# Optimization experiments

Measured on AMD Instinct MI355X. Metric: run time of the kernel, lower is better.

The kernel has to match this reference:

```python
import jax, jax.numpy as jnp
import numpy as np

TS = 1.5          # hard-coded sampling period in forward()
W_CENTER = 337.927  # hard-coded center frequency in forward()


def shg_mat(yta):
    """Vectorized createSHGmat: yta is a complex64 vector of length N.
    Row m: Ts * fftshift(fft(fftshift(yta * roll(yta, delay[m]) * shiftFactor))).
    torch.roll(x, s)[j] == x[(j - s) % N], matching the gather below."""
    N = yta.shape[0]
    delays_f = jnp.arange(-(N // 2), N // 2, dtype=jnp.float32)
    delays_i = jnp.arange(-(N // 2), N // 2, dtype=jnp.int32)
    shift_factor = jnp.exp(-1j * 2.0 * W_CENTER * TS * delays_f).astype(jnp.complex64)  # [N]
    idx = (jnp.arange(N, dtype=jnp.int32)[None, :] - delays_i[:, None]) % N  # [N, N]
    y_shift = yta[idx]                                    # [N(delay), N(elem)]
    prod = yta[None, :] * y_shift * shift_factor[None, :]  # elementwise, [N, N]
    prod = jnp.fft.fftshift(prod, axes=-1)
    mat = TS * jnp.fft.fftshift(jnp.fft.fft(prod, axis=-1), axes=-1)
    return mat  # complex64 [N, N]


def frog_error(Tref, Tmeas):
    """calcFrogError: scalar FROG error between reference and measured traces."""
    mu = jnp.sum(Tmeas @ Tref) / jnp.sum(Tref @ Tref)
    r = jnp.sum((Tmeas - mu * Tref) ** 2)
    norm = jnp.float32(Tmeas.size) * jnp.max(Tmeas) ** 2
    return jnp.sqrt(r / norm)


def setup_inputs() -> dict:
    key = jax.random.key(0)
    k1, k2, k3 = jax.random.split(key, 3)
    B, N = 8, 1024
    prediction = jax.random.normal(k1, (B, 2 * N), dtype=jnp.float32)
    label = jax.random.normal(k2, (B, 2 * N), dtype=jnp.float32)
    spectrogram = jax.random.uniform(k3, (N, N), dtype=jnp.float32)
    return {"prediction": prediction, "label": label, "spectrogram": spectrogram}


def reference(prediction, label, spectrogram):
    B, two_n = prediction.shape
    n = two_n // 2
    pred_analytical = (prediction[:, :n] + 1j * prediction[:, n:]).astype(jnp.complex64)  # [B, N]
    mats = jax.vmap(shg_mat)(pred_analytical)          # [B, N, N] complex64
    Tref = jnp.abs(mats)                               # predicted SHG trace magnitude
    errs = jax.vmap(lambda t: frog_error(t, spectrogram))(Tref)  # [B]
    # loss = (sum over batch of frog_error) / batch_size; masked MSE terms in the
    # original are computed but never added to the returned loss, so they are omitted.
    return jnp.mean(errs)
```

## Files before the change

kernel.cpp:

```cpp
#include <hip/hip_runtime.h>
#include <math.h>

#define N 1024
#define B_ 8
#define T_ 512
#define NREP 4
#define CHUNKS 64

#define OFF_SF      0
#define OFF_TA      2048
#define OFF_TB      4096
#define OFF_ROWSUM  4224
#define ZERO_START  12416
#define OFF_COLSUMM 12416
#define OFF_SUMM2   13440
#define OFF_MAXM    13441
#define OFF_SUMMT   13448
#define OFF_SUMTT   13456
#define OFF_COLT    13464
#define WS_END      (OFF_COLT + B_ * NREP * N)

typedef float f2 __attribute__((ext_vector_type(2)));
__device__ __forceinline__ f2 mkf2(float a, float b) { f2 r; r.x = a; r.y = b; return r; }

__device__ __forceinline__ f2 cmulv(f2 a, f2 b) {
    f2 p = mkf2(a.x, a.x) * b;
    f2 q = mkf2(a.y, a.y) * mkf2(b.y, b.x);
    return mkf2(p.x - q.x, p.y + q.y);
}

__device__ __forceinline__ void dft4v(f2& a0, f2& a1, f2& a2, f2& a3) {
    f2 e0 = a0 + a2, e1 = a0 - a2, e2 = a1 + a3, e3 = a1 - a3;
    a0 = e0 + e2;
    a2 = e0 - e2;
    a1 = mkf2(e1.x + e3.y, e1.y - e3.x);
    a3 = mkf2(e1.x - e3.y, e1.y + e3.x);
}

__device__ __forceinline__ void dft16v(f2 x[16]) {
    #pragma unroll
    for (int b = 0; b < 4; ++b) dft4v(x[b], x[4 + b], x[8 + b], x[12 + b]);
    const float C1 = 0.9238795325112867f, S1 = 0.3826834323650898f;
    const float C2 = 0.7071067811865476f;
    x[5]  = cmulv(x[5],  mkf2( C1, -S1));
    x[6]  = cmulv(x[6],  mkf2( C2, -C2));
    x[7]  = cmulv(x[7],  mkf2( S1, -C1));
    x[9]  = cmulv(x[9],  mkf2( C2, -C2));
    x[10] = mkf2(x[10].y, -x[10].x);
    x[11] = cmulv(x[11], mkf2(-C2, -C2));
    x[13] = cmulv(x[13], mkf2( S1, -C1));
    x[14] = cmulv(x[14], mkf2(-C2, -C2));
    x[15] = cmulv(x[15], mkf2(-C1,  S1));
    #pragma unroll
    for (int c = 0; c < 4; ++c) dft4v(x[4*c], x[4*c+1], x[4*c+2], x[4*c+3]);
}

__device__ __forceinline__ float wave_sum(float v) {
    #pragma unroll
    for (int o = 32; o > 0; o >>= 1) v += __shfl_down(v, o, 64);
    return v;
}
__device__ __forceinline__ float wave_max(float v) {
    #pragma unroll
    for (int o = 32; o > 0; o >>= 1) v = fmaxf(v, __shfl_down(v, o, 64));
    return v;
}

template<int CTRL>
__device__ __forceinline__ float dppf(float x) {
    return __int_as_float(__builtin_amdgcn_update_dpp(
        0, __float_as_int(x), CTRL, 0xF, 0xF, true));
}
#define DPP_XOR1 0xB1
#define DPP_XOR2 0x4E

__global__ __launch_bounds__(256) void k_prep(float* ws) {
    const int e = blockIdx.x * 256 + threadIdx.x;
    if (e < 1024) {
        double ang = -2.0 * 337.927 * 1.5 * (double)(e - 512);
        double s, c;
        sincos(ang, &s, &c);
        ws[OFF_SF + 2 * e]     = (float)c;
        ws[OFF_SF + 2 * e + 1] = (float)s;
    } else if (e < 2048) {
        int e2 = e - 1024;
        int k1 = e2 >> 6, uu = e2 & 63;
        double ang = -2.0 * M_PI * (double)(uu * k1) / 1024.0;
        double s, c;
        sincos(ang, &s, &c);
        ws[OFF_TA + 2 * e2]     = (float)c;
        ws[OFF_TA + 2 * e2 + 1] = (float)s;
    } else if (e < 2112) {
        int e2 = e - 2048;
        int k2 = e2 >> 2, n3 = e2 & 3;
        double ang = -2.0 * M_PI * (double)(n3 * k2) / 64.0;
        double s, c;
        sincos(ang, &s, &c);
        ws[OFF_TB + 2 * e2]     = (float)c;
        ws[OFF_TB + 2 * e2 + 1] = (float)s;
    }
}

__global__ __attribute__((amdgpu_flat_work_group_size(T_, T_), amdgpu_waves_per_eu(2, 4)))
void k_row(const float* __restrict__ pred,
           const float* __restrict__ M,
           float* __restrict__ ws) {
    __shared__ f2   Y2[N];
    __shared__ f2   Ysf[N];
    __shared__ f2   taL[N];
    __shared__ f2   TPh[8][N / 2];
    __shared__ f2   TB2[64];
    __shared__ float colAcc[N];
    __shared__ float redf[2][8];
    const int t = threadIdx.x;
    const int cnk = blockIdx.x;
    const int y = blockIdx.y;
    const int wid = t >> 6, u = t & 63;

    if (y == 0) {
        const int r0 = cnk * 16;
        float cs0 = 0.f, cs1 = 0.f, sq = 0.f, mx = 0.f;
        for (int r = 0; r < 16; ++r) {
            const float* row = M + (size_t)(r0 + r) * N;
            float v0 = row[t], v1 = row[t + 512];
            cs0 += v0; cs1 += v1;
            sq += v0 * v0 + v1 * v1;
            mx = fmaxf(mx, fmaxf(v0, v1));
        }
        atomicAdd(&ws[OFF_COLSUMM + t],       cs0);
        atomicAdd(&ws[OFF_COLSUMM + t + 512], cs1);
        sq = wave_sum(sq);
        mx = wave_max(mx);
        if (u == 0) { redf[0][wid] = sq; redf[1][wid] = mx; }
        __syncthreads();
        if (t == 0) {
            float ssq = 0.f, smx = 0.f;
            #pragma unroll
            for (int i = 0; i < 8; ++i) { ssq += redf[0][i]; smx = fmaxf(smx, redf[1][i]); }
            atomicAdd(&ws[OFF_SUMM2], ssq);
            atomicMax((unsigned int*)ws + OFF_MAXM, __float_as_uint(smx));
        }
        return;
    }
    const int b = y - 1;

    {
        const float* pr = pred + (size_t)b * 2 * N;
        float2 re = *(const float2*)(pr + 2 * t);
        float2 im = *(const float2*)(pr + N + 2 * t);
        const f2* g = (const f2*)ws;
        f2 y0 = mkf2(re.x, im.x), y1 = mkf2(re.y, im.y);
        Y2[2 * t]     = y0;
        Y2[2 * t + 1] = y1;
        Ysf[2 * t]     = cmulv(y0, g[OFF_SF / 2 + 2 * t]);
        Ysf[2 * t + 1] = cmulv(y1, g[OFF_SF / 2 + 2 * t + 1]);
        taL[t]       = g[OFF_TA / 2 + t];
        taL[t + 512] = g[OFF_TA / 2 + t + 512];
        if (t < 64) TB2[t] = g[OFF_TB / 2 + t];
        colAcc[t] = 0.f;
        colAcc[t + 512] = 0.f;
    }
    __syncthreads();

    const int k1u = u >> 2;
    const int n3 = u & 3;
    const int k3 = ((u & 1) << 1) | ((u >> 1) & 1);
    const int clane = (k1u | (k3 << 8)) ^ 512;
    const bool hi2 = (u & 2) != 0;
    const bool odd = (u & 1) != 0;
    f2* tp = TPh[wid];

    float mtl = 0.f, ttl = 0.f;
    const int nrow = (cnk == 0 && wid == 0) ? 2 : 1;

    for (int rr = 0; rr < nrow; ++rr) {
        const int m = (rr == 0) ? (cnk * 8 + wid) : 512;
        const int mm = (N - m) & (N - 1);
        const bool domm = (mm != m);
        const float w = domm ? 2.f : 1.f;
        const float mmw = domm ? 1.f : 0.f;

        f2 x[16];
        const int sbase = (u - m + 512) & (N - 1);
        #pragma unroll
        for (int n1 = 0; n1 < 16; ++n1) {
            int j = (n1 << 6) + u;
            int s = (sbase + (n1 << 6)) & (N - 1);
            x[n1] = cmulv(Ysf[j], Y2[s]);
        }
        dft16v(x);
        #pragma unroll
        for (int r = 1; r < 16; ++r) {
            int k1 = ((r & 3) << 2) | (r >> 2);
            x[r] = cmulv(x[r], taL[(k1 << 6) + u]);
        }

        const float* Mrow  = M + (size_t)m * N + clane;
        const float* Mrow2 = M + (size_t)mm * N + clane;
        float mrA[16], mrB[16];
        #pragma unroll
        for (int r = 0; r < 16; ++r) {
            int k2 = ((r & 3) << 2) | (r >> 2);
            mrA[r] = Mrow[k2 << 4];
        }
        if (domm) {
            #pragma unroll
            for (int r = 0; r < 16; ++r) {
                int k2 = ((r & 3) << 2) | (r >> 2);
                mrB[r] = Mrow2[k2 << 4];
            }
        } else {
            #pragma unroll
            for (int r = 0; r < 16; ++r) mrB[r] = 0.f;
        }

        f2 yv[16];
        asm volatile("s_waitcnt lgkmcnt(0)" ::: "memory");
        #pragma unroll
        for (int r = 0; r < 16; ++r) if ((r & 3) < 2) {
            int k1 = ((r & 3) << 2) | (r >> 2);
            int el = ((k1 & 7) << 6) | (((k1u ^ k1) & 15) << 2) | n3;
            tp[el] = x[r];
        }
        asm volatile("s_waitcnt lgkmcnt(0)" ::: "memory");
        if (u < 32) {
            #pragma unroll
            for (int n2 = 0; n2 < 16; ++n2) {
                int el = ((k1u & 7) << 6) | (((n2 ^ k1u) & 15) << 2) | n3;
                yv[n2] = tp[el];
            }
        }
        asm volatile("s_waitcnt lgkmcnt(0)" ::: "memory");
        #pragma unroll
        for (int r = 0; r < 16; ++r) if ((r & 3) >= 2) {
            int k1 = ((r & 3) << 2) | (r >> 2);
            int el = ((k1 & 7) << 6) | (((k1u ^ k1) & 15) << 2) | n3;
            tp[el] = x[r];
        }
        asm volatile("s_waitcnt lgkmcnt(0)" ::: "memory");
        if (u >= 32) {
            #pragma unroll
            for (int n2 = 0; n2 < 16; ++n2) {
                int el = ((k1u & 7) << 6) | (((n2 ^ k1u) & 15) << 2) | n3;
                yv[n2] = tp[el];
            }
        }

        dft16v(yv);
        #pragma unroll
        for (int r = 1; r < 16; ++r) {
            int k2 = ((r & 3) << 2) | (r >> 2);
            yv[r] = cmulv(yv[r], TB2[(k2 << 2) | n3]);
        }

        const float w225 = w * 2.25f;
        float rs = 0.f;
        #pragma unroll
        for (int r = 0; r < 16; ++r) {
            int k2 = ((r & 3) << 2) | (r >> 2);
            float ar = yv[r].x, ai = yv[r].y;
            float br = dppf<DPP_XOR2>(ar), bi = dppf<DPP_XOR2>(ai);
            float zr = hi2 ? (br - ar) : (ar + br);
            float zi = hi2 ? (bi - ai) : (ai + bi);
            float qr = dppf<DPP_XOR1>(zr), qi = dppf<DPP_XOR1>(zi);
            float Xr = odd ? (qr - (hi2 ? zi : zr)) : (zr + (hi2 ? qi : qr));
            float Xi = odd ? (qi + (hi2 ? zr : -zi)) : (zi + (hi2 ? -qr : qi));
            float mag2 = Xr * Xr + Xi * Xi;
            float v = 1.5f * sqrtf(mag2);
            rs  += v;
            ttl += w225 * mag2;
            float ms = mrA[r] + mmw * mrB[r];
            mtl += ms * v;
            int cc = clane + (k2 << 4);
            atomicAdd(&colAcc[cc ^ ((cc >> 4) & 16)], w * v);
        }
        rs = wave_sum(rs);
        if (u == 0) {
            ws[OFF_ROWSUM + (size_t)b * N + m] = rs;
            if (domm) ws[OFF_ROWSUM + (size_t)b * N + mm] = rs;
        }
    }

    mtl = wave_sum(mtl);
    ttl = wave_sum(ttl);
    if (u == 0) { redf[0][wid] = mtl; redf[1][wid] = ttl; }
    __syncthreads();
    if (t == 0) {
        float smt = 0.f, stt = 0.f;
        #pragma unroll
        for (int i = 0; i < 8; ++i) { smt += redf[0][i]; stt += redf[1][i]; }
        atomicAdd(&ws[OFF_SUMMT + b], smt);
        atomicAdd(&ws[OFF_SUMTT + b], stt);
    }
    {
        float* colT = ws + OFF_COLT + (size_t)(b * NREP + (cnk & (NREP - 1))) * N;
        int j = t;
        atomicAdd(&colT[j], colAcc[j ^ ((j >> 4) & 16)]);
        j = t + 512;
        atomicAdd(&colT[j], colAcc[j ^ ((j >> 4) & 16)]);
    }
}

__global__ __launch_bounds__(256) void k_final(float* ws, float* out) {
    __shared__ double redn[4], redd[4];
    const int b = blockIdx.x;
    const int t = threadIdx.x;
    const int wid = t >> 6, lane = t & 63;
    const float* rowsum = ws + OFF_ROWSUM + (size_t)b * N;
    double num = 0.0, den = 0.0;
    #pragma unroll
    for (int q = 0; q < 4; ++q) {
        int j = t + 256 * q;
        double r = (double)rowsum[j];
        float ct = 0.f;
        #pragma unroll
        for (int rep = 0; rep < NREP; ++rep)
            ct += ws[OFF_COLT + (size_t)(b * NREP + rep) * N + j];
        num += (double)ws[OFF_COLSUMM + j] * r;
        den += (double)ct * r;
    }
    #pragma unroll
    for (int o = 32; o > 0; o >>= 1) {
        num += __shfl_down(num, o, 64);
        den += __shfl_down(den, o, 64);
    }
    if (lane == 0) { redn[wid] = num; redd[wid] = den; }
    __syncthreads();
    if (t == 0) {
        double NUM = redn[0] + redn[1] + redn[2] + redn[3];
        double DEN = redd[0] + redd[1] + redd[2] + redd[3];
        double mu = NUM / DEN;
        double r = (double)ws[OFF_SUMM2] - 2.0 * mu * (double)ws[OFF_SUMMT + b]
                 + mu * mu * (double)ws[OFF_SUMTT + b];
        float mx = ws[OFF_MAXM];
        double norm = 1048576.0 * (double)mx * (double)mx;
        atomicAdd(out, (float)(sqrt(r / norm) / 8.0));
    }
}

extern "C" void kernel_launch(void* const* d_in, const int* in_sizes, int n_in,
                              void* d_out, int out_size, void* d_ws, size_t ws_size,
                              hipStream_t stream) {
    const float* pred = (const float*)d_in[0];
    const float* M = (const float*)d_in[2];
    float* ws = (float*)d_ws;
    float* out = (float*)d_out;

    hipMemsetAsync(ws + ZERO_START, 0, (size_t)(WS_END - ZERO_START) * sizeof(float), stream);
    hipMemsetAsync(out, 0, sizeof(float), stream);
    k_prep<<<9, 256, 0, stream>>>(ws);
    dim3 grid(CHUNKS, B_ + 1);
    k_row<<<grid, T_, 0, stream>>>(pred, M, ws);
    k_final<<<B_, 256, 0, stream>>>(ws, out);
}
```

Before: 107.2 us.

## Fold spectrogram statistics into compute blocks and defer M row loads

Removes the dedicated y==0 block row that computed spectrogram column sums, sum of squares and max. Each of the 512 compute blocks now handles two spectrogram rows at its tail, so the statistics work is spread evenly instead of running in 64 separate blocks. The per-row M loads also move from before the second DFT stage into the magnitude loop, which removes 32 live registers but exposes global load latency at the point of use.

```diff
diff --git a/kernel.cpp b/kernel.cpp
--- a/kernel.cpp
+++ b/kernel.cpp
@@ -114,35 +114,8 @@
     __shared__ float redf[2][8];
     const int t = threadIdx.x;
     const int cnk = blockIdx.x;
-    const int y = blockIdx.y;
+    const int b = blockIdx.y;
     const int wid = t >> 6, u = t & 63;
-
-    if (y == 0) {
-        const int r0 = cnk * 16;
-        float cs0 = 0.f, cs1 = 0.f, sq = 0.f, mx = 0.f;
-        for (int r = 0; r < 16; ++r) {
-            const float* row = M + (size_t)(r0 + r) * N;
-            float v0 = row[t], v1 = row[t + 512];
-            cs0 += v0; cs1 += v1;
-            sq += v0 * v0 + v1 * v1;
-            mx = fmaxf(mx, fmaxf(v0, v1));
-        }
-        atomicAdd(&ws[OFF_COLSUMM + t],       cs0);
-        atomicAdd(&ws[OFF_COLSUMM + t + 512], cs1);
-        sq = wave_sum(sq);
-        mx = wave_max(mx);
-        if (u == 0) { redf[0][wid] = sq; redf[1][wid] = mx; }
-        __syncthreads();
-        if (t == 0) {
-            float ssq = 0.f, smx = 0.f;
-            #pragma unroll
-            for (int i = 0; i < 8; ++i) { ssq += redf[0][i]; smx = fmaxf(smx, redf[1][i]); }
-            atomicAdd(&ws[OFF_SUMM2], ssq);
-            atomicMax((unsigned int*)ws + OFF_MAXM, __float_as_uint(smx));
-        }
-        return;
-    }
-    const int b = y - 1;
 
     {
         const float* pr = pred + (size_t)b * 2 * N;
@@ -195,25 +168,6 @@
             x[r] = cmulv(x[r], taL[(k1 << 6) + u]);
         }
 
-        const float* Mrow  = M + (size_t)m * N + clane;
-        const float* Mrow2 = M + (size_t)mm * N + clane;
-        float mrA[16], mrB[16];
-        #pragma unroll
-        for (int r = 0; r < 16; ++r) {
-            int k2 = ((r & 3) << 2) | (r >> 2);
-            mrA[r] = Mrow[k2 << 4];
-        }
-        if (domm) {
-            #pragma unroll
-            for (int r = 0; r < 16; ++r) {
-                int k2 = ((r & 3) << 2) | (r >> 2);
-                mrB[r] = Mrow2[k2 << 4];
-            }
-        } else {
-            #pragma unroll
-            for (int r = 0; r < 16; ++r) mrB[r] = 0.f;
-        }
-
         f2 yv[16];
         asm volatile("s_waitcnt lgkmcnt(0)" ::: "memory");
         #pragma unroll
@@ -253,6 +207,8 @@
             yv[r] = cmulv(yv[r], TB2[(k2 << 2) | n3]);
         }
 
+        const float* Mrow  = M + (size_t)m * N + clane;
+        const float* Mrow2 = M + (size_t)mm * N + clane;
         const float w225 = w * 2.25f;
         float rs = 0.f;
         #pragma unroll
@@ -269,7 +225,7 @@
             float v = 1.5f * sqrtf(mag2);
             rs  += v;
             ttl += w225 * mag2;
-            float ms = mrA[r] + mmw * mrB[r];
+            float ms = Mrow[k2 << 4] + mmw * Mrow2[k2 << 4];
             mtl += ms * v;
             int cc = clane + (k2 << 4);
             atomicAdd(&colAcc[cc ^ ((cc >> 4) & 16)], w * v);
@@ -298,6 +254,30 @@
         atomicAdd(&colT[j], colAcc[j ^ ((j >> 4) & 16)]);
         j = t + 512;
         atomicAdd(&colT[j], colAcc[j ^ ((j >> 4) & 16)]);
+    }
+
+    {
+        const int gid = b * CHUNKS + cnk;
+        const float* s0 = M + (size_t)(2 * gid) * N;
+        const float* s1 = s0 + N;
+        float a0 = s0[t], a1 = s0[t + 512];
+        float b0 = s1[t], b1 = s1[t + 512];
+        atomicAdd(&ws[OFF_COLSUMM + t],       a0 + b0);
+        atomicAdd(&ws[OFF_COLSUMM + t + 512], a1 + b1);
+        float sq = a0 * a0 + a1 * a1 + b0 * b0 + b1 * b1;
+        float mx = fmaxf(fmaxf(a0, a1), fmaxf(b0, b1));
+        sq = wave_sum(sq);
+        mx = wave_max(mx);
+        __syncthreads();
+        if (u == 0) { redf[0][wid] = sq; redf[1][wid] = mx; }
+        __syncthreads();
+        if (t == 0) {
+            float ssq = 0.f, smx = 0.f;
+            #pragma unroll
+            for (int i = 0; i < 8; ++i) { ssq += redf[0][i]; smx = fmaxf(smx, redf[1][i]); }
+            atomicAdd(&ws[OFF_SUMM2], ssq);
+            atomicMax((unsigned int*)ws + OFF_MAXM, __float_as_uint(smx));
+        }
     }
 }
 
@@ -349,7 +329,7 @@
     hipMemsetAsync(ws + ZERO_START, 0, (size_t)(WS_END - ZERO_START) * sizeof(float), stream);
     hipMemsetAsync(out, 0, sizeof(float), stream);
     k_prep<<<9, 256, 0, stream>>>(ws);
-    dim3 grid(CHUNKS, B_ + 1);
+    dim3 grid(CHUNKS, B_);
     k_row<<<grid, T_, 0, stream>>>(pred, M, ws);
     k_final<<<B_, 256, 0, stream>>>(ws, out);
 }
```

After: 112.6 us. +5.0%, slower.
